# Kernel tuning notes

Hardware: AMD Instinct MI355X
Metric: run time of the kernel (lower is better)

Reference implementation:

```python
import jax, jax.numpy as jnp
import numpy as np

B, N, D = 16, 2048, 1024   # batch, num_windows, input_dim
H, A = 256, 128            # feature head dim, attention hidden dim
EPS = 1e-5                 # torch LayerNorm eps
NEG = -1e9                 # finite mask value (avoids NaN in softmax/grads)
KMAX = max(1, N // 10)     # static upper bound on per-sample top-k


def setup_inputs() -> dict:
    key = jax.random.key(0)
    ks = jax.random.split(key, 6)
    rn = lambda k, shape, sc: jax.random.normal(k, shape, jnp.float32) * sc
    return {
        "x": rn(ks[0], (B, N, D), 1.0),
        "lengths": jax.random.randint(ks[1], (B,), 0, N, dtype=jnp.int64)
                   if jax.config.jax_enable_x64 else
                   jax.random.randint(ks[1], (B,), 0, N, dtype=jnp.int32),
        # feature_head: Linear(D,H) + LayerNorm(H) (+ GELU, dropout=eval no-op)
        "W1": rn(ks[2], (H, D), D ** -0.5), "b1": jnp.zeros((H,), jnp.float32),
        "ln_g": jnp.ones((H,), jnp.float32), "ln_b": jnp.zeros((H,), jnp.float32),
        # attention: Linear(H,A) -> tanh -> Linear(A,1)
        "Wa1": rn(ks[3], (A, H), H ** -0.5), "ba1": jnp.zeros((A,), jnp.float32),
        "Wa2": rn(ks[4], (1, A), A ** -0.5), "ba2": jnp.zeros((1,), jnp.float32),
        # classifier: Linear(H,1)
        "Wc": rn(ks[5], (1, H), H ** -0.5), "bc": jnp.zeros((1,), jnp.float32),
    }


def reference(x, lengths, W1, b1, ln_g, ln_b, Wa1, ba1, Wa2, ba2, Wc, bc):
    # feature head: Linear + LayerNorm + exact GELU (dropout is identity in eval)
    h = jnp.einsum('bnd,hd->bnh', x, W1) + b1
    mu = h.mean(-1, keepdims=True)
    var = h.var(-1, keepdims=True)  # biased, as in torch LayerNorm
    h = (h - mu) * jax.lax.rsqrt(var + EPS) * ln_g + ln_b
    h = jax.nn.gelu(h, approximate=False)

    instance_scores = jnp.einsum('bnh,oh->bno', h, Wc)[..., 0] + bc[0]   # (B, N)
    a_hidden = jnp.tanh(jnp.einsum('bnh,ah->bna', h, Wa1) + ba1)
    attn_logits = jnp.einsum('bna,oa->bno', a_hidden, Wa2)[..., 0] + ba2[0]  # (B, N)

    T = lengths                                    # (B,)
    mask = jnp.arange(N)[None, :] < T[:, None]     # (B, N) valid-window mask

    # masked softmax attention pooling over the first T windows
    w = jax.nn.softmax(jnp.where(mask, attn_logits, NEG), axis=1)
    attn_score = jnp.sum(w * instance_scores * mask, axis=1)

    # dynamic top-k: k = max(1, floor(0.1*T)); take static KMAX then mask ranks
    k_i = jnp.maximum(1, T // 10)                  # (B,)
    vals, _ = jax.lax.top_k(jnp.where(mask, instance_scores, NEG), KMAX)
    rank_mask = jnp.arange(KMAX)[None, :] < k_i[:, None]
    topk_mean = jnp.sum(vals * rank_mask, axis=1) / k_i.astype(vals.dtype)

    video = jnp.where(T > 0, 0.5 * attn_score + 0.5 * topk_mean,
                      jnp.zeros((), vals.dtype))
    return video[:, None], instance_scores
```

## Files before the change

kernel.cpp:

```cpp
#include <hip/hip_runtime.h>
#include <hip/hip_bf16.h>
#include <cmath>

#define Bn 16
#define Nn 2048
#define Dn 1024
#define Hn 256
#define An 128

typedef __bf16 bf16x8 __attribute__((ext_vector_type(8)));
typedef float f32x4 __attribute__((ext_vector_type(4)));
typedef unsigned short ushort8v __attribute__((ext_vector_type(8)));
typedef unsigned int uint4v __attribute__((ext_vector_type(4)));

#define LDS_BARRIER do {                                   \
    asm volatile("s_waitcnt lgkmcnt(0)" ::: "memory");     \
    __builtin_amdgcn_s_barrier();                          \
    __builtin_amdgcn_sched_barrier(0);                     \
  } while (0)

static __device__ __forceinline__ unsigned short f2bf(float f) {
  unsigned u = __float_as_uint(f);
  u += 0x7fffu + ((u >> 16) & 1u);
  return (unsigned short)(u >> 16);
}

static __device__ __forceinline__ bf16x8 cvt8(const float4 a, const float4 b) {
  bf16x8 r;
  r[0] = (__bf16)a.x; r[1] = (__bf16)a.y; r[2] = (__bf16)a.z; r[3] = (__bf16)a.w;
  r[4] = (__bf16)b.x; r[5] = (__bf16)b.y; r[6] = (__bf16)b.z; r[7] = (__bf16)b.w;
  return r;
}

__global__ __launch_bounds__(256) void pack_weights(
    const float* __restrict__ W1, const float* __restrict__ Wa1,
    unsigned short* __restrict__ w1p, unsigned short* __restrict__ wa1p) {
  const int idx = blockIdx.x * 256 + threadIdx.x;
  const float* src;
  unsigned short* dst;
  if (blockIdx.x < 128) {
    const int kc  = idx >> 10;
    const int u   = idx & 1023;
    const int col = u >> 2;
    const int lq  = (u & 3) ^ ((col >> 1) & 3);
    src = W1 + (size_t)col * Dn + (kc << 5) + (lq << 3);
    dst = w1p + (size_t)idx * 8;
  } else {
    const int v   = idx - 32768;
    const int row = v >> 5;
    const int ls  = (v & 31) ^ (row & 7);
    src = Wa1 + (size_t)row * Hn + (ls << 3);
    dst = wa1p + (size_t)v * 8;
  }
  const float4 a = *(const float4*)src;
  const float4 b = *(const float4*)(src + 4);
  ushort8v o;
  o[0] = f2bf(a.x); o[1] = f2bf(a.y); o[2] = f2bf(a.z); o[3] = f2bf(a.w);
  o[4] = f2bf(b.x); o[5] = f2bf(b.y); o[6] = f2bf(b.z); o[7] = f2bf(b.w);
  *(ushort8v*)dst = o;
}

#define K1A(p) ((p) * 16384)
#define K1H    0
#define K1RED  32768
__global__ __launch_bounds__(256, 2) void gemm_ln_kernel(
    const float* __restrict__ x,
    const float* __restrict__ b1,
    const float* __restrict__ ln_g,
    const float* __restrict__ ln_b,
    const float* __restrict__ Wc,
    const float* __restrict__ bc,
    const unsigned short* __restrict__ w1p,
    float* __restrict__ scores_out,
    unsigned short* __restrict__ h_out)
{
  __shared__ __align__(16) char lds[34816];

  const int tid  = threadIdx.x;
  const int wv   = tid >> 6;
  const int lane = tid & 63;
  const int l15  = lane & 15;
  const int lhi  = lane >> 4;
  const int rg   = wv >> 1;
  const int cw   = wv & 1;

  const int gr0 = blockIdx.x << 6;
  const int bb  = gr0 >> 11;
  const int n0  = gr0 & (Nn - 1);

  f32x4 acc[2][8];
  #pragma unroll
  for (int rf = 0; rf < 2; ++rf)
    #pragma unroll
    for (int cf = 0; cf < 8; ++cf)
      acc[rf][cf] = (f32x4){0.f, 0.f, 0.f, 0.f};

  const int arow = tid >> 2, akq = tid & 3;
  const float* xsrc = x + (size_t)(gr0 + arow) * Dn + (akq << 5);

  const int ar0 = (rg << 5) + l15;
  const int ar1 = ar0 + 16;
  const int axk = l15 & 7;

  const int pq = lhi ^ ((l15 >> 1) & 3);
  const unsigned short* bbase = w1p + (((cw << 7) + l15) << 5) + (pq << 3);

  float4 ast[8];
  bf16x8 Bpre[2][8];

  auto loadA = [&](int ch) {
    #pragma unroll
    for (int j = 0; j < 8; ++j)
      ast[j] = *(const float4*)(xsrc + (ch << 7) + (j << 2));
  };
  auto writeA = [&](int p) {
    #pragma unroll
    for (int j = 0; j < 4; ++j)
      *(bf16x8*)(lds + K1A(p) + arow * 256 +
                 ((((akq << 2) + j) ^ (arow & 7)) << 4)) = cvt8(ast[2 * j], ast[2 * j + 1]);
  };
  auto loadB = [&](bf16x8* dst, int kc) {
    #pragma unroll
    for (int cf = 0; cf < 8; ++cf)
      dst[cf] = *(const bf16x8*)(bbase + (size_t)kc * 8192 + (cf << 9));
  };
  auto computeStep = [&](const bf16x8* Bf, int p, int s) {
    const char* Ab = lds + K1A(p);
    const int sx = ((((s << 2) + lhi) ^ axk) << 4);
    const bf16x8 a0 = *(const bf16x8*)(Ab + ar0 * 256 + sx);
    const bf16x8 a1 = *(const bf16x8*)(Ab + ar1 * 256 + sx);
    __builtin_amdgcn_s_setprio(1);
    #pragma unroll
    for (int cf = 0; cf < 8; ++cf) {
      acc[0][cf] = __builtin_amdgcn_mfma_f32_16x16x32_bf16(a0, Bf[cf], acc[0][cf], 0, 0, 0);
      acc[1][cf] = __builtin_amdgcn_mfma_f32_16x16x32_bf16(a1, Bf[cf], acc[1][cf], 0, 0, 0);
    }
    __builtin_amdgcn_s_setprio(0);
  };

  loadA(0);
  writeA(0);
  loadB(Bpre[0], 0);
  loadB(Bpre[1], 1);
  LDS_BARRIER;
  loadA(1);

  #pragma unroll 1
  for (int ch = 0; ch < 8; ++ch) {
    const int cb = ch & 1;
    #pragma unroll
    for (int s = 0; s < 4; ++s) {
      const int kc = (ch << 2) + s;
      computeStep(Bpre[s & 1], cb, s);
      if (kc < 30) loadB(Bpre[s & 1], kc + 2);
    }
    if (ch < 7) {
      writeA(cb ^ 1);
      LDS_BARRIER;
      if (ch < 6) loadA(ch + 2);
    }
  }
  __syncthreads();

  float (*red)[8] = (float(*)[8])(lds + K1RED);

  const float bc0 = bc[0];
  float b1v[8];
  #pragma unroll
  for (int cf = 0; cf < 8; ++cf) b1v[cf] = b1[(cw << 7) + (cf << 4) + l15];

  float ps[2][4], ps2[2][4];
  #pragma unroll
  for (int rf = 0; rf < 2; ++rf)
    #pragma unroll
    for (int r = 0; r < 4; ++r) { ps[rf][r] = 0.f; ps2[rf][r] = 0.f; }

  #pragma unroll
  for (int rf = 0; rf < 2; ++rf)
    #pragma unroll
    for (int cf = 0; cf < 8; ++cf)
      #pragma unroll
      for (int r = 0; r < 4; ++r) {
        const float v = acc[rf][cf][r] + b1v[cf];
        acc[rf][cf][r] = v;
        ps[rf][r] += v; ps2[rf][r] += v * v;
      }
  #pragma unroll
  for (int rf = 0; rf < 2; ++rf)
    #pragma unroll
    for (int r = 0; r < 4; ++r)
      #pragma unroll
      for (int s = 1; s < 16; s <<= 1) {
        ps[rf][r]  += __shfl_xor(ps[rf][r],  s, 64);
        ps2[rf][r] += __shfl_xor(ps2[rf][r], s, 64);
      }
  if (l15 == 0) {
    #pragma unroll
    for (int rf = 0; rf < 2; ++rf)
      #pragma unroll
      for (int r = 0; r < 4; ++r) {
        const int rowb = (rg << 5) + (rf << 4) + (lhi << 2) + r;
        red[rowb][cw << 1]       = ps[rf][r];
        red[rowb][(cw << 1) + 1] = ps2[rf][r];
      }
  }
  __syncthreads();

  float mu[2][4], inv[2][4];
  #pragma unroll
  for (int rf = 0; rf < 2; ++rf)
    #pragma unroll
    for (int r = 0; r < 4; ++r) {
      const int rowb = (rg << 5) + (rf << 4) + (lhi << 2) + r;
      const float s = red[rowb][0] + red[rowb][2];
      const float q = red[rowb][1] + red[rowb][3];
      const float m = s * (1.f / 256.f);
      const float var = q * (1.f / 256.f) - m * m;
      mu[rf][r] = m;
      inv[rf][r] = rsqrtf(var + 1e-5f);
    }

  float gv[8], bv[8], wcv[8];
  #pragma unroll
  for (int cf = 0; cf < 8; ++cf) {
    const int col = (cw << 7) + (cf << 4) + l15;
    gv[cf] = ln_g[col]; bv[cf] = ln_b[col]; wcv[cf] = Wc[col];
  }
  float sc[2][4];
  #pragma unroll
  for (int rf = 0; rf < 2; ++rf)
    #pragma unroll
    for (int r = 0; r < 4; ++r) sc[rf][r] = 0.f;

  #pragma unroll
  for (int rf = 0; rf < 2; ++rf)
    #pragma unroll
    for (int cf = 0; cf < 8; ++cf)
      #pragma unroll
      for (int r = 0; r < 4; ++r) {
        float v = (acc[rf][cf][r] - mu[rf][r]) * inv[rf][r] * gv[cf] + bv[cf];
        v = 0.5f * v * (1.f + erff(v * 0.70710678118654752f));
        sc[rf][r] += v * wcv[cf];
        const int rowb = (rg << 5) + (rf << 4) + (lhi << 2) + r;
        const int col  = (cw << 7) + (cf << 4) + l15;
        *(__bf16*)(lds + K1H + rowb * 512 + (((col >> 3) ^ (rowb & 7)) << 4)
                   + ((col & 7) << 1)) = (__bf16)v;
      }
  #pragma unroll
  for (int rf = 0; rf < 2; ++rf)
    #pragma unroll
    for (int r = 0; r < 4; ++r)
      #pragma unroll
      for (int s = 1; s < 16; s <<= 1)
        sc[rf][r] += __shfl_xor(sc[rf][r], s, 64);
  if (l15 == 0) {
    #pragma unroll
    for (int rf = 0; rf < 2; ++rf)
      #pragma unroll
      for (int r = 0; r < 4; ++r) {
        const int rowb = (rg << 5) + (rf << 4) + (lhi << 2) + r;
        red[rowb][4 + cw] = sc[rf][r];
      }
  }
  __syncthreads();
  if (tid < 64)
    scores_out[(size_t)bb * Nn + n0 + tid] = red[tid][4] + red[tid][5] + bc0;

  #pragma unroll
  for (int j = 0; j < 8; ++j) {
    const int g   = (j << 8) + tid;
    const int row = g >> 5;
    const int c   = g & 31;
    const bf16x8 hv = *(const bf16x8*)(lds + K1H + row * 512 +
                                       ((c ^ (row & 7)) << 4));
    *(bf16x8*)(h_out + (size_t)(gr0 + row) * 256 + (c << 3)) = hv;
  }
}

__global__ __launch_bounds__(512) void stage2_kernel(
    const unsigned short* __restrict__ h_in,
    const unsigned short* __restrict__ wa1p,
    const float* __restrict__ ba1,
    const float* __restrict__ Wa2,
    const float* __restrict__ ba2,
    float* __restrict__ logits_out)
{
  __shared__ __align__(16) char lds2[65536];

  const int tid  = threadIdx.x;
  const int wv   = tid >> 6;
  const int lane = tid & 63;
  const int l15  = lane & 15;
  const int lhi  = lane >> 4;

  const int gr0 = blockIdx.x << 7;
  const int bb  = gr0 >> 11;
  const int n0  = gr0 & (Nn - 1);

  {
    uint4v st[8];
    #pragma unroll
    for (int j = 0; j < 8; ++j)
      st[j] = *(const uint4v*)(wa1p + (size_t)((j << 9) + tid) * 8);
    #pragma unroll
    for (int j = 0; j < 8; ++j)
      *(uint4v*)(lds2 + ((j << 9) + tid) * 16) = st[j];
  }
  __syncthreads();

  f32x4 acc2[8];
  #pragma unroll
  for (int cf = 0; cf < 8; ++cf) acc2[cf] = (f32x4){0.f, 0.f, 0.f, 0.f};

  const unsigned short* hrow = h_in + (size_t)(gr0 + (wv << 4) + l15) * 256 + (lhi << 3);
  #pragma unroll
  for (int ks = 0; ks < 8; ++ks) {
    const bf16x8 af = *(const bf16x8*)(hrow + (ks << 5));
    #pragma unroll
    for (int cf = 0; cf < 8; ++cf) {
      const int row2 = (cf << 4) + l15;
      const bf16x8 bfr = *(const bf16x8*)(lds2 + row2 * 512 +
                          ((((ks << 2) + lhi) ^ (row2 & 7)) << 4));
      acc2[cf] = __builtin_amdgcn_mfma_f32_16x16x32_bf16(af, bfr, acc2[cf], 0, 0, 0);
    }
  }
  const float ba20 = ba2[0];
  float lg[4] = {0.f, 0.f, 0.f, 0.f};
  #pragma unroll
  for (int cf = 0; cf < 8; ++cf) {
    const int col = (cf << 4) + l15;
    const float bav = ba1[col], w2v = Wa2[col];
    #pragma unroll
    for (int r = 0; r < 4; ++r) {
      const float t = acc2[cf][r] + bav;
      const float e = __expf(2.f * t);
      const float th = 1.f - 2.f / (e + 1.f);
      lg[r] += th * w2v;
    }
  }
  #pragma unroll
  for (int r = 0; r < 4; ++r)
    #pragma unroll
    for (int s = 1; s < 16; s <<= 1) lg[r] += __shfl_xor(lg[r], s, 64);
  if (l15 == 0) {
    #pragma unroll
    for (int r = 0; r < 4; ++r)
      logits_out[(size_t)bb * Nn + n0 + (wv << 4) + (lhi << 2) + r] = lg[r] + ba20;
  }
}

__global__ __launch_bounds__(256) void finalize_kernel(
    const int* __restrict__ lengths,
    const float* __restrict__ scores,
    const float* __restrict__ logits,
    float* __restrict__ video)
{
  const int b = blockIdx.x;
  const int tid = threadIdx.x;
  __shared__ float sS[Nn];
  __shared__ float sL[Nn];
  __shared__ unsigned skey[Nn];
  __shared__ float sred[8];

  const int T = lengths[b];
  for (int i = tid; i < Nn; i += 256) {
    sS[i] = scores[(size_t)b * Nn + i];
    sL[i] = logits[(size_t)b * Nn + i];
  }
  __syncthreads();
  if (T <= 0) { if (tid == 0) video[b] = 0.f; return; }

  float m = -3.0e38f;
  for (int i = tid; i < T; i += 256) m = fmaxf(m, sL[i]);
  #pragma unroll
  for (int s = 1; s < 64; s <<= 1) m = fmaxf(m, __shfl_xor(m, s, 64));
  if ((tid & 63) == 0) sred[tid >> 6] = m;
  __syncthreads();
  m = fmaxf(fmaxf(sred[0], sred[1]), fmaxf(sred[2], sred[3]));
  __syncthreads();

  float se = 0.f, swe = 0.f;
  for (int i = tid; i < T; i += 256) {
    const float e = expf(sL[i] - m);
    se += e; swe += e * sS[i];
  }
  #pragma unroll
  for (int s = 1; s < 64; s <<= 1) { se += __shfl_xor(se, s, 64); swe += __shfl_xor(swe, s, 64); }
  if ((tid & 63) == 0) { sred[tid >> 6] = se; sred[4 + (tid >> 6)] = swe; }
  __syncthreads();
  se  = sred[0] + sred[1] + sred[2] + sred[3];
  swe = sred[4] + sred[5] + sred[6] + sred[7];
  __syncthreads();
  const float attn = swe / se;

  for (int i = tid; i < T; i += 256) {
    const unsigned u = __float_as_uint(sS[i]);
    skey[i] = (u & 0x80000000u) ? ~u : (u | 0x80000000u);
  }
  __syncthreads();
  const int k = max(1, T / 10);
  unsigned ans = 0u;
  for (int bit = 31; bit >= 0; --bit) {
    const unsigned cand = ans | (1u << bit);
    int c = 0;
    for (int i = tid; i < T; i += 256) c += (skey[i] >= cand) ? 1 : 0;
    #pragma unroll
    for (int s = 1; s < 64; s <<= 1) c += __shfl_xor(c, s, 64);
    if ((tid & 63) == 0) sred[tid >> 6] = (float)c;
    __syncthreads();
    c = (int)(sred[0] + sred[1] + sred[2] + sred[3]);
    __syncthreads();
    if (c >= k) ans = cand;
  }
  int cgt = 0; float sgt = 0.f;
  for (int i = tid; i < T; i += 256) {
    if (skey[i] > ans) { cgt++; sgt += sS[i]; }
  }
  #pragma unroll
  for (int s = 1; s < 64; s <<= 1) { cgt += __shfl_xor(cgt, s, 64); sgt += __shfl_xor(sgt, s, 64); }
  if ((tid & 63) == 0) { sred[tid >> 6] = (float)cgt; sred[4 + (tid >> 6)] = sgt; }
  __syncthreads();
  cgt = (int)(sred[0] + sred[1] + sred[2] + sred[3]);
  sgt = sred[4] + sred[5] + sred[6] + sred[7];

  const unsigned ub = (ans & 0x80000000u) ? (ans ^ 0x80000000u) : ~ans;
  const float kth = __uint_as_float(ub);
  const float topk = (sgt + (float)(k - cgt) * kth) / (float)k;
  if (tid == 0) video[b] = 0.5f * attn + 0.5f * topk;
}

extern "C" void kernel_launch(void* const* d_in, const int* in_sizes, int n_in,
                              void* d_out, int out_size, void* d_ws, size_t ws_size,
                              hipStream_t stream) {
  const float* x    = (const float*)d_in[0];
  const int*   len  = (const int*)  d_in[1];
  const float* W1   = (const float*)d_in[2];
  const float* b1   = (const float*)d_in[3];
  const float* ln_g = (const float*)d_in[4];
  const float* ln_b = (const float*)d_in[5];
  const float* Wa1  = (const float*)d_in[6];
  const float* ba1  = (const float*)d_in[7];
  const float* Wa2  = (const float*)d_in[8];
  const float* ba2  = (const float*)d_in[9];
  const float* Wc   = (const float*)d_in[10];
  const float* bc   = (const float*)d_in[11];

  float* out    = (float*)d_out;
  float* video  = out;
  float* scores = out + Bn;

  char* ws = (char*)d_ws;
  float*          logits = (float*)ws;
  unsigned short* h_g    = (unsigned short*)(ws + 131072);
  unsigned short* w1p    = (unsigned short*)(ws + 131072 + 16777216);
  unsigned short* wa1p   = (unsigned short*)(ws + 131072 + 16777216 + 524288);

  hipLaunchKernelGGL(pack_weights, dim3(144), dim3(256), 0, stream, W1, Wa1, w1p, wa1p);
  hipLaunchKernelGGL(gemm_ln_kernel, dim3(Bn * Nn / 64), dim3(256), 0, stream,
                     x, b1, ln_g, ln_b, Wc, bc, w1p, scores, h_g);
  hipLaunchKernelGGL(stage2_kernel, dim3(Bn * Nn / 128), dim3(512), 0, stream,
                     h_g, wa1p, ba1, Wa2, ba2, logits);
  hipLaunchKernelGGL(finalize_kernel, dim3(Bn), dim3(256), 0, stream, len, scores, logits, video);
}
```

Measured before the change: 95.90 us.

## Fuse attention-hidden GEMM into feature GEMM kernel, dropping h round-trip

Merges the second stage (h·Wa1ᵀ, tanh, Wa2 dot) into the first GEMM+LayerNorm kernel. The LayerNorm/GELU output h now stays in LDS and Wa1 is read directly from global memory, instead of being written to and reloaded from a 16 MB bf16 buffer. It also adds sched_barriers around the load/compute steps of the main loop to pin instruction ordering. The trade-offs are Wa1 B-fragment reads from global/L2 with no LDS staging, and a longer tail in each block of the first kernel. The remaining stage-2 tail code (wave/row mapping for 64-row blocks with 4 waves) must be consistent with the new block shape.

```diff
diff --git a/kernel.cpp b/kernel.cpp
--- a/kernel.cpp
+++ b/kernel.cpp
@@ -11,7 +11,6 @@
 typedef __bf16 bf16x8 __attribute__((ext_vector_type(8)));
 typedef float f32x4 __attribute__((ext_vector_type(4)));
 typedef unsigned short ushort8v __attribute__((ext_vector_type(8)));
-typedef unsigned int uint4v __attribute__((ext_vector_type(4)));
 
 #define LDS_BARRIER do {                                   \
     asm volatile("s_waitcnt lgkmcnt(0)" ::: "memory");     \
@@ -63,16 +62,20 @@
 #define K1A(p) ((p) * 16384)
 #define K1H    0
 #define K1RED  32768
-__global__ __launch_bounds__(256, 2) void gemm_ln_kernel(
+__global__ __launch_bounds__(256, 2) void fused_main(
     const float* __restrict__ x,
     const float* __restrict__ b1,
     const float* __restrict__ ln_g,
     const float* __restrict__ ln_b,
     const float* __restrict__ Wc,
     const float* __restrict__ bc,
+    const float* __restrict__ ba1,
+    const float* __restrict__ Wa2,
+    const float* __restrict__ ba2,
     const unsigned short* __restrict__ w1p,
+    const unsigned short* __restrict__ wa1p,
     float* __restrict__ scores_out,
-    unsigned short* __restrict__ h_out)
+    float* __restrict__ logits_out)
 {
   __shared__ __align__(16) char lds[34816];
 
@@ -142,8 +145,10 @@
   writeA(0);
   loadB(Bpre[0], 0);
   loadB(Bpre[1], 1);
+  __builtin_amdgcn_sched_barrier(0);
   LDS_BARRIER;
   loadA(1);
+  __builtin_amdgcn_sched_barrier(0);
 
   #pragma unroll 1
   for (int ch = 0; ch < 8; ++ch) {
@@ -152,12 +157,18 @@
     for (int s = 0; s < 4; ++s) {
       const int kc = (ch << 2) + s;
       computeStep(Bpre[s & 1], cb, s);
-      if (kc < 30) loadB(Bpre[s & 1], kc + 2);
+      if (kc < 30) {
+        loadB(Bpre[s & 1], kc + 2);
+        __builtin_amdgcn_sched_barrier(0);
+      }
     }
     if (ch < 7) {
       writeA(cb ^ 1);
       LDS_BARRIER;
-      if (ch < 6) loadA(ch + 2);
+      if (ch < 6) {
+        loadA(ch + 2);
+        __builtin_amdgcn_sched_barrier(0);
+      }
     }
   }
   __syncthreads();
@@ -266,61 +277,20 @@
   if (tid < 64)
     scores_out[(size_t)bb * Nn + n0 + tid] = red[tid][4] + red[tid][5] + bc0;
 
-  #pragma unroll
-  for (int j = 0; j < 8; ++j) {
-    const int g   = (j << 8) + tid;
-    const int row = g >> 5;
-    const int c   = g & 31;
-    const bf16x8 hv = *(const bf16x8*)(lds + K1H + row * 512 +
-                                       ((c ^ (row & 7)) << 4));
-    *(bf16x8*)(h_out + (size_t)(gr0 + row) * 256 + (c << 3)) = hv;
-  }
-}
-
-__global__ __launch_bounds__(512) void stage2_kernel(
-    const unsigned short* __restrict__ h_in,
-    const unsigned short* __restrict__ wa1p,
-    const float* __restrict__ ba1,
-    const float* __restrict__ Wa2,
-    const float* __restrict__ ba2,
-    float* __restrict__ logits_out)
-{
-  __shared__ __align__(16) char lds2[65536];
-
-  const int tid  = threadIdx.x;
-  const int wv   = tid >> 6;
-  const int lane = tid & 63;
-  const int l15  = lane & 15;
-  const int lhi  = lane >> 4;
-
-  const int gr0 = blockIdx.x << 7;
-  const int bb  = gr0 >> 11;
-  const int n0  = gr0 & (Nn - 1);
-
-  {
-    uint4v st[8];
-    #pragma unroll
-    for (int j = 0; j < 8; ++j)
-      st[j] = *(const uint4v*)(wa1p + (size_t)((j << 9) + tid) * 8);
-    #pragma unroll
-    for (int j = 0; j < 8; ++j)
-      *(uint4v*)(lds2 + ((j << 9) + tid) * 16) = st[j];
-  }
-  __syncthreads();
-
   f32x4 acc2[8];
   #pragma unroll
   for (int cf = 0; cf < 8; ++cf) acc2[cf] = (f32x4){0.f, 0.f, 0.f, 0.f};
 
-  const unsigned short* hrow = h_in + (size_t)(gr0 + (wv << 4) + l15) * 256 + (lhi << 3);
+  const int r16 = (wv << 4) + l15;
   #pragma unroll
   for (int ks = 0; ks < 8; ++ks) {
-    const bf16x8 af = *(const bf16x8*)(hrow + (ks << 5));
+    const bf16x8 af = *(const bf16x8*)(lds + K1H + r16 * 512 +
+                        ((((ks << 2) + lhi) ^ (r16 & 7)) << 4));
     #pragma unroll
     for (int cf = 0; cf < 8; ++cf) {
       const int row2 = (cf << 4) + l15;
-      const bf16x8 bfr = *(const bf16x8*)(lds2 + row2 * 512 +
-                          ((((ks << 2) + lhi) ^ (row2 & 7)) << 4));
+      const bf16x8 bfr = *(const bf16x8*)(wa1p + (size_t)row2 * 256 +
+                          ((((ks << 2) + lhi) ^ (row2 & 7)) << 3));
       acc2[cf] = __builtin_amdgcn_mfma_f32_16x16x32_bf16(af, bfr, acc2[cf], 0, 0, 0);
     }
   }
@@ -451,14 +421,12 @@
 
   char* ws = (char*)d_ws;
   float*          logits = (float*)ws;
-  unsigned short* h_g    = (unsigned short*)(ws + 131072);
-  unsigned short* w1p    = (unsigned short*)(ws + 131072 + 16777216);
-  unsigned short* wa1p   = (unsigned short*)(ws + 131072 + 16777216 + 524288);
+  unsigned short* w1p    = (unsigned short*)(ws + 131072);
+  unsigned short* wa1p   = (unsigned short*)(ws + 131072 + 524288);
 
   hipLaunchKernelGGL(pack_weights, dim3(144), dim3(256), 0, stream, W1, Wa1, w1p, wa1p);
-  hipLaunchKernelGGL(gemm_ln_kernel, dim3(Bn * Nn / 64), dim3(256), 0, stream,
-                     x, b1, ln_g, ln_b, Wc, bc, w1p, scores, h_g);
-  hipLaunchKernelGGL(stage2_kernel, dim3(Bn * Nn / 128), dim3(512), 0, stream,
-                     h_g, wa1p, ba1, Wa2, ba2, logits);
+  hipLaunchKernelGGL(fused_main, dim3(Bn * Nn / 64), dim3(256), 0, stream,
+                     x, b1, ln_g, ln_b, Wc, bc, ba1, Wa2, ba2,
+                     w1p, wa1p, scores, logits);
   hipLaunchKernelGGL(finalize_kernel, dim3(Bn), dim3(256), 0, stream, len, scores, logits, video);
 }
```

Result: faster. 91.76 us (-4.3%).
